# Optimization experiments

Hardware: AMD Instinct MI355X
Metric: run time of the kernel (lower is better)

## Reference

```python
import jax, jax.numpy as jnp
import numpy as np

S = 41          # seq_len
D_IN = 1280
D_OUT = 1024
HEADS = 4
HC = D_OUT // HEADS
EPS = 1e-5

# ---- static edge construction (faithful to the torch code, incl. duplicate edges) ----

def _local_edges(s, window=1):
    e = []
    for i in range(s):
        for j in range(max(0, i - window), min(s, i + window + 1)):
            if i != j:
                e += [(i, j), (j, i)]
    return np.array(e, dtype=np.int32).T

def _region_edges(s):
    e = []
    step = s // 3
    for st in range(0, s, step):
        blk = range(st, min(st + step, s))
        for i in blk:
            for j in blk:
                if i != j:
                    e += [(i, j), (j, i)]
    return np.array(e, dtype=np.int32).T

def _global_edges(s):
    r, c = np.triu_indices(s, 1)  # torch.combinations: (i, j) with i < j
    return np.stack([r, c]).astype(np.int32)

def _batch_edges(e, b, s):
    off = np.arange(b, dtype=np.int32) * s
    return (e[:, None, :] + off[None, :, None]).reshape(2, -1)

_LOCAL = _local_edges(S)
_REGION = _region_edges(S)
_GLOBAL = _global_edges(S)

# ---- layer primitives ----

def _layernorm(x, g, b):
    mu = x.mean(-1, keepdims=True)
    v = ((x - mu) ** 2).mean(-1, keepdims=True)
    return (x - mu) / jnp.sqrt(v + EPS) * g + b

def _gcn(x, w, b, src, tgt, n):
    # PyG GCNConv: x' = D^-1/2 (A + I) D^-1/2 (x W) + b
    h = x @ w
    sl = jnp.arange(n, dtype=src.dtype)
    s = jnp.concatenate([src, sl]); t = jnp.concatenate([tgt, sl])
    deg = jax.ops.segment_sum(jnp.ones(t.shape, h.dtype), t, n)
    dinv = jnp.where(deg > 0, jax.lax.rsqrt(jnp.maximum(deg, 1.0)), 0.0)
    norm = dinv[s] * dinv[t]
    return jax.ops.segment_sum(h[s] * norm[:, None], t, n) + b

def _gat(x, w, a_src, a_dst, b, src, tgt, n):
    # PyG GATConv (shared lin, self loops, leaky_relu 0.2, softmax over incoming edges)
    h = (x @ w).reshape(n, HEADS, HC)
    sl = jnp.arange(n, dtype=src.dtype)
    s = jnp.concatenate([src, sl]); t = jnp.concatenate([tgt, sl])
    al_s = (h * a_src).sum(-1)  # [n, H]
    al_d = (h * a_dst).sum(-1)
    e = jax.nn.leaky_relu(al_s[s] + al_d[t], 0.2)  # [E, H]
    m = jax.ops.segment_max(e, t, n)
    ex = jnp.exp(e - m[t])
    den = jax.ops.segment_sum(ex, t, n)
    alpha = ex / den[t]
    out = jax.ops.segment_sum(h[s] * alpha[:, :, None], t, n)
    return out.reshape(n, HEADS * HC) + b

def _sage(x, wl, bl, wr, src, tgt, n):
    # PyG SAGEConv: mean-aggregate neighbors, plus root transform
    cnt = jax.ops.segment_sum(jnp.ones(src.shape, x.dtype), tgt, n)
    agg = jax.ops.segment_sum(x[src], tgt, n) / jnp.maximum(cnt, 1.0)[:, None]
    return agg @ wl + bl + x @ wr


def setup_inputs() -> dict:
    key = jax.random.key(0)
    ks = jax.random.split(key, 16)
    sc = 0.02
    f32 = jnp.float32
    inp = {
        'x': jax.random.normal(ks[0], (512, S, D_IN), f32),
        'att_w': jax.random.normal(ks[1], (D_IN, 1), f32) * sc,
        'att_b': jnp.zeros((1,), f32),
        'gcn_w': jax.random.normal(ks[2], (D_IN, D_OUT), f32) * sc,
        'gcn_b': jnp.zeros((D_OUT,), f32),
        'sn_g': jnp.ones((D_OUT,), f32), 'sn_b': jnp.zeros((D_OUT,), f32),
        'gat_w': jax.random.normal(ks[3], (D_IN, D_OUT), f32) * sc,
        'gat_as': jax.random.normal(ks[4], (HEADS, HC), f32) * sc,
        'gat_ad': jax.random.normal(ks[5], (HEADS, HC), f32) * sc,
        'gat_b': jnp.zeros((D_OUT,), f32),
        'mn_g': jnp.ones((D_OUT,), f32), 'mn_b': jnp.zeros((D_OUT,), f32),
        'sage_wl': jax.random.normal(ks[6], (D_IN, D_OUT), f32) * sc,
        'sage_bl': jnp.zeros((D_OUT,), f32),
        'sage_wr': jax.random.normal(ks[7], (D_IN, D_OUT), f32) * sc,
        'fp_w1': jax.random.normal(ks[8], (D_IN, 512), f32) * sc,
        'fp_b1': jnp.zeros((512,), f32),
        'fp_w2': jax.random.normal(ks[9], (512, S), f32) * sc,
        'fp_b2': jnp.zeros((S,), f32),
        'dn_g': jnp.ones((D_OUT,), f32), 'dn_b': jnp.zeros((D_OUT,), f32),
        'gate_w': jax.random.normal(ks[10], (3 * D_OUT, 3), f32) * sc,
        'gate_b': jnp.zeros((3,), f32),
    }
    return inp


def reference(x, att_w, att_b, gcn_w, gcn_b, sn_g, sn_b, gat_w, gat_as, gat_ad, gat_b,
              mn_g, mn_b, sage_wl, sage_bl, sage_wr, fp_w1, fp_b1, fp_w2, fp_b2,
              dn_g, dn_b, gate_w, gate_b):
    B = x.shape[0]
    N = B * S
    le = jnp.asarray(_batch_edges(_LOCAL, B, S))
    re = jnp.asarray(_batch_edges(_REGION, B, S))
    ge = jnp.asarray(_batch_edges(_GLOBAL, B, S))

    xf = x.reshape(N, D_IN)
    # shallow: local gating -> GCN -> LN
    enhanced = xf * jax.nn.sigmoid(xf @ att_w + att_b)
    shallow = _gcn(enhanced, gcn_w, gcn_b, le[0], le[1], N)
    shallow = _layernorm(shallow.reshape(B, S, D_OUT), sn_g, sn_b)
    # medium: GAT over region blocks -> LN
    gat = _gat(xf, gat_w, gat_as[None], gat_ad[None], gat_b, re[0], re[1], N)
    gat = _layernorm(gat.reshape(B, S, D_OUT), mn_g, mn_b)
    # deep: learned propagation mixing, SAGE over global edges -> LN
    pw = jax.nn.softmax(jax.nn.relu(x @ fp_w1 + fp_b1) @ fp_w2 + fp_b2, axis=-1)  # [B,S,S]
    sage_in = jnp.einsum('bij,bjd->bid', pw, x).reshape(N, D_IN)
    sage = _sage(sage_in, sage_wl, sage_bl, sage_wr, ge[0], ge[1], N)
    sage = _layernorm(sage.reshape(B, S, D_OUT), dn_g, dn_b)
    # gated branch mixing
    combined = jnp.concatenate([shallow, gat, sage], axis=-1)
    gates = jax.nn.softmax(combined @ gate_w + gate_b, axis=-1)
    total = gates[..., 0:1] * shallow + gates[..., 1:2] * gat + gates[..., 2:3] * sage
    return (shallow, gat, total)
```

## Files before the change

### kernel.cpp

```cpp
#include <hip/hip_runtime.h>
#include <math.h>

static constexpr int S    = 41;
static constexpr int DIN  = 1280;
static constexpr int DOUT = 1024;
static constexpr int HEADS = 4;
static constexpr int HC   = 256;

typedef __attribute__((ext_vector_type(4))) float f32x4;
typedef __attribute__((ext_vector_type(8))) short short8;

__device__ __forceinline__ ushort f2bf(float f) {
  uint u = __float_as_uint(f);
  uint r = u + 0x7fffu + ((u >> 16) & 1u);
  return (ushort)(r >> 16);
}
__device__ __forceinline__ float bf2f(ushort u) {
  return __uint_as_float(((uint)u) << 16);
}

__device__ __forceinline__ void gload16(const ushort* g, ushort* l) {
  __builtin_amdgcn_global_load_lds((const __attribute__((address_space(1))) void*)g,
                                   (__attribute__((address_space(3))) void*)l, 16, 0, 0);
}

#define FENCE() asm volatile("" ::: "memory")


__device__ __forceinline__ float warpReduceSum(float v) {
#pragma unroll
  for (int off = 32; off; off >>= 1) v += __shfl_down(v, off);
  return v;
}


__global__ __launch_bounds__(256) void cvtsig_kernel(
    const float4* __restrict__ x, const float* __restrict__ att_w,
    const float* __restrict__ att_b, ushort4* __restrict__ xb, float* __restrict__ sig)
{
  int row  = blockIdx.x * 4 + (threadIdx.x >> 6);
  int lane = threadIdx.x & 63;
  const float4* xr = x + (size_t)row * (DIN / 4);
  const float4* wr = (const float4*)att_w;
  ushort4* xo = xb + (size_t)row * (DIN / 4);
  float acc = 0.f;
#pragma unroll
  for (int k = 0; k < DIN / 4 / 64; ++k) {
    float4 a = xr[lane + k * 64];
    float4 w = wr[lane + k * 64];
    acc += a.x * w.x + a.y * w.y + a.z * w.z + a.w * w.w;
    ushort4 o;
    o.x = f2bf(a.x); o.y = f2bf(a.y); o.z = f2bf(a.z); o.w = f2bf(a.w);
    xo[lane + k * 64] = o;
  }
  acc = warpReduceSum(acc);
  if (lane == 0) sig[row] = 1.f / (1.f + expf(-(acc + att_b[0])));
}


struct W4 { const float* src[4]; ushort* dst[4]; };

__global__ __launch_bounds__(256) void wcvt4_kernel(W4 w) {
  __shared__ float t[32][33];
  const float* W = w.src[blockIdx.z];
  ushort* out = w.dst[blockIdx.z];
  int n0 = blockIdx.x * 32, k0 = blockIdx.y * 32;
  int tx = threadIdx.x & 31, ty = threadIdx.x >> 5;
#pragma unroll
  for (int r = 0; r < 4; ++r) {
    int k = ty + r * 8;
    t[k][tx] = W[(size_t)(k0 + k) * DOUT + n0 + tx];
  }
  __syncthreads();
#pragma unroll
  for (int r = 0; r < 4; ++r) {
    int nn = ty + r * 8;
    out[(size_t)(n0 + nn) * DIN + k0 + tx] = f2bf(t[tx][nn]);
  }
}

__global__ __launch_bounds__(256) void wcvt_kernel(const float* __restrict__ W,
                                                   ushort* __restrict__ out,
                                                   int K, int N, int ostride, int koff) {
  __shared__ float t[32][33];
  int n0 = blockIdx.x * 32, k0 = blockIdx.y * 32;
  int tx = threadIdx.x & 31, ty = threadIdx.x >> 5;
#pragma unroll
  for (int r = 0; r < 4; ++r) {
    int k = ty + r * 8;
    t[k][tx] = W[(size_t)(k0 + k) * N + n0 + tx];
  }
  __syncthreads();
#pragma unroll
  for (int r = 0; r < 4; ++r) {
    int nn = ty + r * 8;
    out[(size_t)(n0 + nn) * ostride + koff + k0 + tx] = f2bf(t[tx][nn]);
  }
}

__global__ __launch_bounds__(256) void w2cvt_kernel(const float* __restrict__ w2,
                                                    ushort* __restrict__ wpw) {
  int idx = blockIdx.x * 256 + threadIdx.x;
  int n = idx >> 9, k = idx & 511;
  wpw[idx] = (n < S) ? f2bf(w2[(size_t)k * S + n]) : (ushort)0;
}


struct Epi {
  void* dst[5];
  const float* bias[5];
  int nend[5];
  int ld[5];
  int relu[5];
  const float* rs;
};


__global__ __launch_bounds__(512, 1) void gemm8p(
    const ushort* __restrict__ A, const ushort* __restrict__ Bt, int K, int nb, Epi e)
{
  __shared__ __align__(16) ushort As[4 * 8192];
  __shared__ __align__(16) ushort Bs[4 * 8192];

  int wg;
  {
    const int nwg = gridDim.x;
    const int bid = blockIdx.x;
    const int xcd = bid & 7, lin = bid >> 3;
    const int q = nwg >> 3, r = nwg & 7;
    wg = (xcd < r) ? (xcd * (q + 1) + lin) : (r * (q + 1) + (xcd - r) * q + lin);
  }
  const int bm = (wg / nb) * 256;
  const int bn = (wg % nb) * 256;

  const int tid  = threadIdx.x;
  const int wv   = tid >> 6;
  const int lane = tid & 63;
  const int l16  = lane & 15;
  const int l4   = lane >> 4;
  const int m0   = (wv >> 2) * 128;
  const int n0   = (wv & 3) * 64;

  const int rd0 = wv * 16 + (lane >> 2);
  const int rd1 = 128 + wv * 16 + (lane >> 2);
  const int cs0 = ((lane & 3) - ((rd0 >> 1) & 3)) & 3;
  const int cs1 = ((lane & 3) - ((rd1 >> 1) & 3)) & 3;

  const ushort* gA0 = A  + (size_t)(bm + rd0) * K + cs0 * 8;
  const ushort* gA1 = A  + (size_t)(bm + rd1) * K + cs1 * 8;
  const ushort* gB0 = Bt + (size_t)(bn + rd0) * K + cs0 * 8;
  const ushort* gB1 = Bt + (size_t)(bn + rd1) * K + cs1 * 8;

  auto stageA = [&](int h, int kof) {
    gload16(gA0 + kof, &As[h * 8192 + wv * 512]);
    gload16(gA1 + kof, &As[h * 8192 + (8 + wv) * 512]);
  };
  auto stageB = [&](int h, int kof) {
    gload16(gB0 + kof, &Bs[h * 8192 + wv * 512]);
    gload16(gB1 + kof, &Bs[h * 8192 + (8 + wv) * 512]);
  };

  const int rchunk = ((l4 + ((l16 >> 1) & 3)) & 3) * 8;

  f32x4 acc[8][4];
#pragma unroll
  for (int i = 0; i < 8; ++i)
#pragma unroll
    for (int j = 0; j < 4; ++j) acc[i][j] = (f32x4)0.f;

  const int NT = K >> 6;

  stageA(0, 0);  stageB(0, 0);
  stageA(1, 32); stageB(1, 32);
  stageA(2, 64); stageB(2, 64);
  asm volatile("s_waitcnt vmcnt(8)" ::: "memory");
  __builtin_amdgcn_s_barrier();
  FENCE();

  auto tileBody = [&](int T, const int db) {
    const int hA = db * 2;
    const int hB = db * 2 + 1;
    short8 a[4], b[4];

#pragma unroll
    for (int i = 0; i < 4; ++i)
      a[i] = *reinterpret_cast<const short8*>(&As[hA * 8192 + (m0 + i * 16 + l16) * 32 + rchunk]);
#pragma unroll
    for (int j = 0; j < 4; ++j)
      b[j] = *reinterpret_cast<const short8*>(&Bs[hA * 8192 + (n0 + j * 16 + l16) * 32 + rchunk]);
    if (T + 1 < NT) stageA((db ^ 1) * 2 + 1, (T + 1) * 64 + 32);
    FENCE(); __builtin_amdgcn_s_barrier(); FENCE();
    __builtin_amdgcn_s_setprio(1);
#pragma unroll
    for (int i = 0; i < 4; ++i)
#pragma unroll
      for (int j = 0; j < 4; ++j)
        acc[i][j] = __builtin_amdgcn_mfma_f32_16x16x32_bf16(a[i], b[j], acc[i][j], 0, 0, 0);
    __builtin_amdgcn_s_setprio(0);
    FENCE(); __builtin_amdgcn_s_barrier(); FENCE();

#pragma unroll
    for (int i = 0; i < 4; ++i)
      a[i] = *reinterpret_cast<const short8*>(&As[hA * 8192 + (m0 + 64 + i * 16 + l16) * 32 + rchunk]);
    if (T + 1 < NT) {
      stageB((db ^ 1) * 2 + 1, (T + 1) * 64 + 32);
      asm volatile("s_waitcnt vmcnt(8)" ::: "memory");
    } else {
      asm volatile("s_waitcnt vmcnt(0)" ::: "memory");
    }
    FENCE(); __builtin_amdgcn_s_barrier(); FENCE();
    __builtin_amdgcn_s_setprio(1);
#pragma unroll
    for (int i = 0; i < 4; ++i)
#pragma unroll
      for (int j = 0; j < 4; ++j)
        acc[4 + i][j] = __builtin_amdgcn_mfma_f32_16x16x32_bf16(a[i], b[j], acc[4 + i][j], 0, 0, 0);
    __builtin_amdgcn_s_setprio(0);
    FENCE(); __builtin_amdgcn_s_barrier(); FENCE();

#pragma unroll
    for (int i = 0; i < 4; ++i)
      a[i] = *reinterpret_cast<const short8*>(&As[hB * 8192 + (m0 + i * 16 + l16) * 32 + rchunk]);
#pragma unroll
    for (int j = 0; j < 4; ++j)
      b[j] = *reinterpret_cast<const short8*>(&Bs[hB * 8192 + (n0 + j * 16 + l16) * 32 + rchunk]);
    if (T + 2 < NT) stageA(hA, (T + 2) * 64);
    FENCE(); __builtin_amdgcn_s_barrier(); FENCE();
    __builtin_amdgcn_s_setprio(1);
#pragma unroll
    for (int i = 0; i < 4; ++i)
#pragma unroll
      for (int j = 0; j < 4; ++j)
        acc[i][j] = __builtin_amdgcn_mfma_f32_16x16x32_bf16(a[i], b[j], acc[i][j], 0, 0, 0);
    __builtin_amdgcn_s_setprio(0);
    FENCE(); __builtin_amdgcn_s_barrier(); FENCE();

#pragma unroll
    for (int i = 0; i < 4; ++i)
      a[i] = *reinterpret_cast<const short8*>(&As[hB * 8192 + (m0 + 64 + i * 16 + l16) * 32 + rchunk]);
    if (T + 2 < NT) {
      stageB(hA, (T + 2) * 64);
      asm volatile("s_waitcnt vmcnt(8)" ::: "memory");
    } else if (T + 1 < NT) {
      asm volatile("s_waitcnt vmcnt(4)" ::: "memory");
    }
    FENCE(); __builtin_amdgcn_s_barrier(); FENCE();
    __builtin_amdgcn_s_setprio(1);
#pragma unroll
    for (int i = 0; i < 4; ++i)
#pragma unroll
      for (int j = 0; j < 4; ++j)
        acc[4 + i][j] = __builtin_amdgcn_mfma_f32_16x16x32_bf16(a[i], b[j], acc[4 + i][j], 0, 0, 0);
    __builtin_amdgcn_s_setprio(0);
    FENCE(); __builtin_amdgcn_s_barrier(); FENCE();
  };

  for (int T = 0; T < NT; T += 2) {
    tileBody(T, 0);
    tileBody(T + 1, 1);
  }

  void* dstv; const float* bias; const float* rs = nullptr; int ldc, cb, relu;
  if (bn < e.nend[0])      { dstv = e.dst[0]; ldc = e.ld[0]; cb = bn;             bias = e.bias[0]; relu = e.relu[0]; rs = e.rs; }
  else if (bn < e.nend[1]) { dstv = e.dst[1]; ldc = e.ld[1]; cb = bn - e.nend[0]; bias = e.bias[1]; relu = e.relu[1]; }
  else if (bn < e.nend[2]) { dstv = e.dst[2]; ldc = e.ld[2]; cb = bn - e.nend[1]; bias = e.bias[2]; relu = e.relu[2]; }
  else if (bn < e.nend[3]) { dstv = e.dst[3]; ldc = e.ld[3]; cb = bn - e.nend[2]; bias = e.bias[3]; relu = e.relu[3]; }
  else                     { dstv = e.dst[4]; ldc = e.ld[4]; cb = bn - e.nend[3]; bias = e.bias[4]; relu = e.relu[4]; }

#pragma unroll
  for (int i = 0; i < 8; ++i) {
    int mbase = bm + m0 + i * 16 + l4 * 4;
    float rsv[4];
#pragma unroll
    for (int r = 0; r < 4; ++r) rsv[r] = rs ? rs[mbase + r] : 1.f;
#pragma unroll
    for (int j = 0; j < 4; ++j) {
      int col = cb + n0 + j * 16 + l16;
      float bv = bias ? bias[col] : 0.f;
#pragma unroll
      for (int r = 0; r < 4; ++r) {
        float t = acc[i][j][r] * rsv[r] + bv;
        if (relu) t = fmaxf(t, 0.f);
        ((ushort*)dstv)[(size_t)(mbase + r) * ldc + col] = f2bf(t);
      }
    }
  }
}


template<bool F32OUT>
__global__ __launch_bounds__(256) void gemm_bf16(
    const ushort* __restrict__ A, const ushort* __restrict__ Bt, int K, int nb, Epi e)
{
  __shared__ __align__(16) ushort As[3][128 * 32];
  __shared__ __align__(16) ushort Bs[3][128 * 32];

  const int bid = blockIdx.x;
  const int bm  = (bid / nb) * 128;
  const int bn  = (bid % nb) * 128;

  const int tid  = threadIdx.x;
  const int w    = tid >> 6;
  const int lane = tid & 63;
  const int l16  = lane & 15;
  const int l4   = lane >> 4;
  const int m0   = (w >> 1) * 64;
  const int n0   = (w & 1) * 64;

  const int rloc = lane >> 2;
  const int cpos = lane & 3;
  const int cdat = (cpos - (rloc >> 1)) & 3;
  const int srow = w * 32 + rloc;
  const int scol = cdat * 8;

  f32x4 acc[4][4];
#pragma unroll
  for (int i = 0; i < 4; ++i)
#pragma unroll
    for (int j = 0; j < 4; ++j) acc[i][j] = (f32x4)0.f;

  const ushort* pA0 = A  + (size_t)(bm + srow) * K + scol;
  const ushort* pA1 = A  + (size_t)(bm + srow + 16) * K + scol;
  const ushort* pB0 = Bt + (size_t)(bn + srow) * K + scol;
  const ushort* pB1 = Bt + (size_t)(bn + srow + 16) * K + scol;

  auto stage = [&](int buf, int kt) {
    gload16(pA0 + kt, &As[buf][w * 1024]);
    gload16(pA1 + kt, &As[buf][w * 1024 + 512]);
    gload16(pB0 + kt, &Bs[buf][w * 1024]);
    gload16(pB1 + kt, &Bs[buf][w * 1024 + 512]);
  };

  const int rchunk = ((l4 + (l16 >> 1)) & 3) * 8;

  const int nsteps = K >> 5;
  stage(0, 0); stage(1, 32); stage(2, 64);

  for (int t = 0; t < nsteps; ++t) {
    if (t == 0)                asm volatile("s_waitcnt vmcnt(8)" ::: "memory");
    else if (t == nsteps - 1)  asm volatile("s_waitcnt vmcnt(0)" ::: "memory");
    else                       asm volatile("s_waitcnt vmcnt(4)" ::: "memory");
    __builtin_amdgcn_s_barrier();
    FENCE();

    if (t >= 1 && t + 2 < nsteps) stage((t + 2) % 3, (t + 2) * 32);

    const int cur = t % 3;
    short8 a[4], b[4];
#pragma unroll
    for (int i = 0; i < 4; ++i)
      a[i] = *reinterpret_cast<const short8*>(&As[cur][(m0 + i * 16 + l16) * 32 + rchunk]);
#pragma unroll
    for (int j = 0; j < 4; ++j)
      b[j] = *reinterpret_cast<const short8*>(&Bs[cur][(n0 + j * 16 + l16) * 32 + rchunk]);
    __builtin_amdgcn_s_setprio(1);
#pragma unroll
    for (int i = 0; i < 4; ++i)
#pragma unroll
      for (int j = 0; j < 4; ++j)
        acc[i][j] = __builtin_amdgcn_mfma_f32_16x16x32_bf16(a[i], b[j], acc[i][j], 0, 0, 0);
    __builtin_amdgcn_s_setprio(0);
  }

  void* dstv; const float* bias; const float* rs = nullptr; int ldc, cb, relu;
  if (bn < e.nend[0])      { dstv = e.dst[0]; ldc = e.ld[0]; cb = bn;             bias = e.bias[0]; relu = e.relu[0]; rs = e.rs; }
  else if (bn < e.nend[1]) { dstv = e.dst[1]; ldc = e.ld[1]; cb = bn - e.nend[0]; bias = e.bias[1]; relu = e.relu[1]; }
  else if (bn < e.nend[2]) { dstv = e.dst[2]; ldc = e.ld[2]; cb = bn - e.nend[1]; bias = e.bias[2]; relu = e.relu[2]; }
  else if (bn < e.nend[3]) { dstv = e.dst[3]; ldc = e.ld[3]; cb = bn - e.nend[2]; bias = e.bias[3]; relu = e.relu[3]; }
  else                     { dstv = e.dst[4]; ldc = e.ld[4]; cb = bn - e.nend[3]; bias = e.bias[4]; relu = e.relu[4]; }

#pragma unroll
  for (int i = 0; i < 4; ++i) {
    int mbase = bm + m0 + i * 16 + l4 * 4;
    float rsv[4];
#pragma unroll
    for (int r = 0; r < 4; ++r) rsv[r] = rs ? rs[mbase + r] : 1.f;
#pragma unroll
    for (int j = 0; j < 4; ++j) {
      int col = cb + n0 + j * 16 + l16;
      float bv = bias ? bias[col] : 0.f;
#pragma unroll
      for (int r = 0; r < 4; ++r) {
        float t = acc[i][j][r] * rsv[r] + bv;
        if (relu) t = fmaxf(t, 0.f);
        if (F32OUT) ((float*)dstv)[(size_t)(mbase + r) * ldc + col] = t;
        else        ((ushort*)dstv)[(size_t)(mbase + r) * ldc + col] = f2bf(t);
      }
    }
  }
}


__global__ __launch_bounds__(256) void pwprep_kernel(
    const float* __restrict__ fp2, const float* __restrict__ fp_b2,
    float* __restrict__ pc)
{
  int b = blockIdx.x;
  int tid = threadIdx.x, wv = tid >> 6, lane = tid & 63;
  __shared__ float pws[S][S];
  for (int i = wv; i < S; i += 4) {
    float v = (lane < S) ? (fp2[(size_t)(b * S + i) * 128 + lane] + fp_b2[lane]) : -1e30f;
    float m = v;
#pragma unroll
    for (int off = 32; off; off >>= 1) m = fmaxf(m, __shfl_xor(m, off));
    float e = (lane < S) ? expf(v - m) : 0.f;
    float sum = e;
#pragma unroll
    for (int off = 32; off; off >>= 1) sum += __shfl_xor(sum, off);
    if (lane < S) {
      float p = e / sum;
      pws[i][lane] = p;
      pc[((size_t)b * S + i) * 128 + lane] = p;
    }
  }
  __syncthreads();
  if (tid < S) {
    float run = 0.f;
    for (int i = 0; i < S; ++i) {
      pc[((size_t)b * S + i) * 128 + 64 + tid] = (i > 0) ? run / (float)i : 0.f;
      run += pws[i][tid];
    }
  }
}


__global__ __launch_bounds__(256) void mixc_kernel(
    const float* __restrict__ pc, const ushort* __restrict__ xr,
    const ushort* __restrict__ xl, const float* __restrict__ sage_bl,
    ushort* __restrict__ hbuf)
{
  int b  = blockIdx.y;
  int d0 = blockIdx.x * 256;
  int tid = threadIdx.x;

  float xrv[S], xlv[S];
  const ushort* xrp = xr + (size_t)(b * S) * DOUT + d0 + tid;
  const ushort* xlp = xl + (size_t)(b * S) * DOUT + d0 + tid;
#pragma unroll
  for (int j = 0; j < S; ++j) {
    xrv[j] = bf2f(xrp[(size_t)j * DOUT]);
    xlv[j] = bf2f(xlp[(size_t)j * DOUT]);
  }
  float bl = sage_bl[d0 + tid];
  ushort* op = hbuf + (size_t)(b * S) * DOUT + d0 + tid;
  const float* pcb = pc + (size_t)(b * S) * 128;
  for (int i = 0; i < S; ++i) {
    const float* row = pcb + (size_t)i * 128;
    float acc = bl;
#pragma unroll
    for (int j = 0; j < S; ++j)
      acc += row[j] * xrv[j] + row[64 + j] * xlv[j];
    op[(size_t)i * DOUT] = f2bf(acc);
  }
}


__device__ __forceinline__ float dinv_local(int j) {
  return rsqrtf((j == 0 || j == S - 1) ? 3.f : 5.f);
}

__global__ __launch_bounds__(256) void tail_fused(
    const ushort* __restrict__ gcnh, const ushort* __restrict__ Cgat,
    const ushort* __restrict__ hbuf,
    const float* __restrict__ gcn_b, const float* __restrict__ sn_g, const float* __restrict__ sn_b,
    const float* __restrict__ gat_as, const float* __restrict__ gat_ad, const float* __restrict__ gat_b,
    const float* __restrict__ mn_g, const float* __restrict__ mn_b,
    const float* __restrict__ dn_g, const float* __restrict__ dn_b,
    const float* __restrict__ gw, const float* __restrict__ gb,
    float* __restrict__ out, int N)
{
  int b  = blockIdx.x >> 2;
  int rb = blockIdx.x & 3;
  int lo = rb * 13;
  int cnt = (rb < 3) ? 13 : 2;
  size_t OUT = (size_t)N * DOUT;
  int tid = threadIdx.x;
  int wv = tid >> 6, lane = tid & 63;
  int d0 = tid * 4;
  int head = tid >> 6;

  __shared__ __align__(16) ushort hs[13][DOUT];
  __shared__ float alpha[13][13][HEADS];
  __shared__ float als_l[13][HEADS], ald_l[13][HEADS];
  __shared__ float red6[2][6][4];
  __shared__ float red3[2][3][4];

  for (int r = 0; r < cnt; ++r) {
    const ushort4* src = (const ushort4*)(Cgat + (size_t)(b * S + lo + r) * DOUT);
    ((ushort4*)hs[r])[tid] = src[tid];
  }
  __syncthreads();

  {
    const float4* a4 = (const float4*)(gat_as + wv * HC);
    const float4* d4 = (const float4*)(gat_ad + wv * HC);
    float4 av = a4[lane], dv = d4[lane];
    for (int s = 0; s < cnt; ++s) {
      ushort4 hv4 = ((const ushort4*)&hs[s][wv * HC])[lane];
      float h0 = bf2f(hv4.x), h1 = bf2f(hv4.y), h2 = bf2f(hv4.z), h3 = bf2f(hv4.w);
      float a = h0 * av.x + h1 * av.y + h2 * av.z + h3 * av.w;
      float d = h0 * dv.x + h1 * dv.y + h2 * dv.z + h3 * dv.w;
      a = warpReduceSum(a);
      d = warpReduceSum(d);
      if (lane == 0) { als_l[s][wv] = a; ald_l[s][wv] = d; }
    }
  }
  __syncthreads();

  if (tid < cnt * HEADS) {
    int t = tid >> 2, hd = tid & 3;
    float myald = ald_l[t][hd];
    float m = -1e30f;
    for (int s = 0; s < cnt; ++s) {
      float v = als_l[s][hd] + myald;
      v = (v > 0.f) ? v : 0.2f * v;
      m = fmaxf(m, v);
    }
    float den = 0.f;
    for (int s = 0; s < cnt; ++s) {
      float v = als_l[s][hd] + myald;
      v = (v > 0.f) ? v : 0.2f * v;
      float ev = expf(v - m) * ((s == t) ? 1.f : 2.f);
      alpha[t][s][hd] = ev;
      den += ev;
    }
    float inv = 1.f / den;
    for (int s = 0; s < cnt; ++s) alpha[t][s][hd] *= inv;
  }
  __syncthreads();

  float4 gcnb4 = *(const float4*)(gcn_b + d0);
  float4 sng4  = *(const float4*)(sn_g + d0);
  float4 snb4  = *(const float4*)(sn_b + d0);
  float4 gatb4 = *(const float4*)(gat_b + d0);
  float4 mng4  = *(const float4*)(mn_g + d0);
  float4 mnb4  = *(const float4*)(mn_b + d0);
  float4 dng4  = *(const float4*)(dn_g + d0);
  float4 dnb4  = *(const float4*)(dn_b + d0);
  float gwsh[4][3], gwga[4][3], gwsa[4][3];
#pragma unroll
  for (int q = 0; q < 4; ++q)
#pragma unroll
    for (int c = 0; c < 3; ++c) {
      gwsh[q][c] = gw[(size_t)(d0 + q) * 3 + c];
      gwga[q][c] = gw[(size_t)(DOUT + d0 + q) * 3 + c];
      gwsa[q][c] = gw[(size_t)(2 * DOUT + d0 + q) * 3 + c];
    }

  for (int t = 0; t < cnt; ++t) {
    int i = lo + t;
    size_t n = (size_t)(b * S + i);
    int par = t & 1;

    float di = dinv_local(i);
    float wc = di * di;
    float wl = (i > 0)     ? 2.f * di * dinv_local(i - 1) : 0.f;
    float wr = (i < S - 1) ? 2.f * di * dinv_local(i + 1) : 0.f;
    const ushort* hc = gcnh + n * DOUT + d0;
    ushort4 c4  = *(const ushort4*)hc;
    ushort4 lft = (i > 0)     ? *(const ushort4*)(hc - DOUT) : ushort4{0, 0, 0, 0};
    ushort4 rgt = (i < S - 1) ? *(const ushort4*)(hc + DOUT) : ushort4{0, 0, 0, 0};
    const ushort* cp = (const ushort*)&c4;
    const ushort* lp = (const ushort*)&lft;
    const ushort* rp = (const ushort*)&rgt;
    const float* gbp = (const float*)&gcnb4;
    float sh[4];
#pragma unroll
    for (int q = 0; q < 4; ++q)
      sh[q] = wc * bf2f(cp[q]) + wl * bf2f(lp[q]) + wr * bf2f(rp[q]) + gbp[q];

    float ga[4] = {0.f, 0.f, 0.f, 0.f};
    for (int si = 0; si < cnt; ++si) {
      float aj = alpha[t][si][head];
      ushort4 hv = *(const ushort4*)&hs[si][d0];
      ga[0] += aj * bf2f(hv.x);
      ga[1] += aj * bf2f(hv.y);
      ga[2] += aj * bf2f(hv.z);
      ga[3] += aj * bf2f(hv.w);
    }
    const float* gab = (const float*)&gatb4;
#pragma unroll
    for (int q = 0; q < 4; ++q) ga[q] += gab[q];

    ushort4 s4v = *(const ushort4*)(hbuf + n * DOUT + d0);
    const ushort* sp = (const ushort*)&s4v;
    float sa[4];
#pragma unroll
    for (int q = 0; q < 4; ++q) sa[q] = bf2f(sp[q]);

    float red[6] = {0.f, 0.f, 0.f, 0.f, 0.f, 0.f};
#pragma unroll
    for (int q = 0; q < 4; ++q) {
      red[0] += sh[q]; red[1] += sh[q] * sh[q];
      red[2] += ga[q]; red[3] += ga[q] * ga[q];
      red[4] += sa[q]; red[5] += sa[q] * sa[q];
    }
#pragma unroll
    for (int r = 0; r < 6; ++r) red[r] = warpReduceSum(red[r]);
    if (lane == 0) {
#pragma unroll
      for (int r = 0; r < 6; ++r) red6[par][r][wv] = red[r];
    }
    __syncthreads();
#pragma unroll
    for (int r = 0; r < 6; ++r)
      red[r] = red6[par][r][0] + red6[par][r][1] + red6[par][r][2] + red6[par][r][3];

    float mu0 = red[0] * (1.f / DOUT), r0 = rsqrtf(red[1] * (1.f / DOUT) - mu0 * mu0 + 1e-5f);
    float mu1 = red[2] * (1.f / DOUT), r1 = rsqrtf(red[3] * (1.f / DOUT) - mu1 * mu1 + 1e-5f);
    float mu2 = red[4] * (1.f / DOUT), r2 = rsqrtf(red[5] * (1.f / DOUT) - mu2 * mu2 + 1e-5f);

    const float* sngp = (const float*)&sng4; const float* snbp = (const float*)&snb4;
    const float* mngp = (const float*)&mng4; const float* mnbp = (const float*)&mnb4;
    const float* dngp = (const float*)&dng4; const float* dnbp = (const float*)&dnb4;
    float shn[4], gan[4], san[4];
#pragma unroll
    for (int q = 0; q < 4; ++q) {
      shn[q] = (sh[q] - mu0) * r0 * sngp[q] + snbp[q];
      gan[q] = (ga[q] - mu1) * r1 * mngp[q] + mnbp[q];
      san[q] = (sa[q] - mu2) * r2 * dngp[q] + dnbp[q];
    }

    float p[3] = {0.f, 0.f, 0.f};
#pragma unroll
    for (int q = 0; q < 4; ++q) {
#pragma unroll
      for (int c = 0; c < 3; ++c)
        p[c] += shn[q] * gwsh[q][c] + gan[q] * gwga[q][c] + san[q] * gwsa[q][c];
    }
#pragma unroll
    for (int r = 0; r < 3; ++r) p[r] = warpReduceSum(p[r]);
    if (lane == 0) {
#pragma unroll
      for (int r = 0; r < 3; ++r) red3[par][r][wv] = p[r];
    }
    __syncthreads();
#pragma unroll
    for (int r = 0; r < 3; ++r)
      p[r] = red3[par][r][0] + red3[par][r][1] + red3[par][r][2] + red3[par][r][3];

    float l0 = p[0] + gb[0], l1 = p[1] + gb[1], l2 = p[2] + gb[2];
    float m = fmaxf(l0, fmaxf(l1, l2));
    float e0 = expf(l0 - m), e1 = expf(l1 - m), e2 = expf(l2 - m);
    float inv = 1.f / (e0 + e1 + e2);
    float g0 = e0 * inv, g1 = e1 * inv, g2 = e2 * inv;

    float4 o0, o1, o2;
    float* o0p = (float*)&o0; float* o1p = (float*)&o1; float* o2p = (float*)&o2;
#pragma unroll
    for (int q = 0; q < 4; ++q) {
      o0p[q] = shn[q];
      o1p[q] = gan[q];
      o2p[q] = g0 * shn[q] + g1 * gan[q] + g2 * san[q];
    }
    *(float4*)(out + n * DOUT + d0)           = o0;
    *(float4*)(out + OUT + n * DOUT + d0)     = o1;
    *(float4*)(out + 2 * OUT + n * DOUT + d0) = o2;
  }
}


extern "C" void kernel_launch(void* const* d_in, const int* in_sizes, int n_in,
                              void* d_out, int out_size, void* d_ws, size_t ws_size,
                              hipStream_t stream) {
  const float* x       = (const float*)d_in[0];
  const float* att_w   = (const float*)d_in[1];
  const float* att_b   = (const float*)d_in[2];
  const float* gcn_w   = (const float*)d_in[3];
  const float* gcn_b   = (const float*)d_in[4];
  const float* sn_g    = (const float*)d_in[5];
  const float* sn_b    = (const float*)d_in[6];
  const float* gat_w   = (const float*)d_in[7];
  const float* gat_as  = (const float*)d_in[8];
  const float* gat_ad  = (const float*)d_in[9];
  const float* gat_b   = (const float*)d_in[10];
  const float* mn_g    = (const float*)d_in[11];
  const float* mn_b    = (const float*)d_in[12];
  const float* sage_wl = (const float*)d_in[13];
  const float* sage_bl = (const float*)d_in[14];
  const float* sage_wr = (const float*)d_in[15];
  const float* fp_w1   = (const float*)d_in[16];
  const float* fp_b1   = (const float*)d_in[17];
  const float* fp_w2   = (const float*)d_in[18];
  const float* fp_b2   = (const float*)d_in[19];
  const float* dn_g    = (const float*)d_in[20];
  const float* dn_b    = (const float*)d_in[21];
  const float* gate_w  = (const float*)d_in[22];
  const float* gate_b  = (const float*)d_in[23];

  const int B = in_sizes[0] / (S * DIN);
  const int N = B * S;
  const int MB  = N / 128;
  const int MB2 = N / 256;
  const int NMEGA = 4608;
  float* out = (float*)d_out;

  char* ws = (char*)d_ws;
  size_t off = 0;
  auto alloc = [&](size_t bytes) { size_t p = off; off += (bytes + 255) & ~(size_t)255; return p; };
  ushort* xb   = (ushort*)(ws + alloc((size_t)N * DIN * 2));
  ushort* Bt   = (ushort*)(ws + alloc((size_t)NMEGA * DIN * 2));
  ushort* wpw  = (ushort*)(ws + alloc((size_t)128 * 512 * 2));
  ushort* gcnh = (ushort*)(ws + alloc((size_t)N * DOUT * 2));
  ushort* Cgat = (ushort*)(ws + alloc((size_t)N * DOUT * 2));
  ushort* xr   = (ushort*)(ws + alloc((size_t)N * DOUT * 2));
  ushort* xl   = (ushort*)(ws + alloc((size_t)N * DOUT * 2));
  ushort* hbuf = (ushort*)(ws + alloc((size_t)N * DOUT * 2));
  float*  fp2  = (float*)(ws + alloc((size_t)N * 128 * 4));
  float*  pc   = (float*)(ws + alloc((size_t)N * 128 * 4));
  float*  sig  = (float*)(ws + alloc((size_t)N * 4));
  ushort* fp1  = hbuf;

  dim3 blk(256);

  cvtsig_kernel<<<N / 4, blk, 0, stream>>>((const float4*)x, att_w, att_b, (ushort4*)xb, sig);
  W4 w4;
  w4.src[0] = gcn_w;  w4.dst[0] = Bt;
  w4.src[1] = gat_w;  w4.dst[1] = Bt + (size_t)1024 * DIN;
  w4.src[2] = sage_wr; w4.dst[2] = Bt + (size_t)2560 * DIN;
  w4.src[3] = sage_wl; w4.dst[3] = Bt + (size_t)3584 * DIN;
  wcvt4_kernel<<<dim3(DOUT / 32, DIN / 32, 4), blk, 0, stream>>>(w4);
  wcvt_kernel<<<dim3(512 / 32, DIN / 32), blk, 0, stream>>>(fp_w1, Bt + (size_t)2048 * DIN, DIN, 512, DIN, 0);
  w2cvt_kernel<<<dim3(128 * 512 / 256), blk, 0, stream>>>(fp_w2, wpw);

  Epi e1;
  e1.dst[0] = gcnh; e1.dst[1] = Cgat; e1.dst[2] = fp1; e1.dst[3] = xr; e1.dst[4] = xl;
  e1.bias[0] = nullptr; e1.bias[1] = nullptr; e1.bias[2] = fp_b1; e1.bias[3] = nullptr; e1.bias[4] = nullptr;
  e1.nend[0] = 1024; e1.nend[1] = 2048; e1.nend[2] = 2560; e1.nend[3] = 3584; e1.nend[4] = 4608;
  e1.ld[0] = DOUT; e1.ld[1] = DOUT; e1.ld[2] = 512; e1.ld[3] = DOUT; e1.ld[4] = DOUT;
  e1.relu[0] = 0; e1.relu[1] = 0; e1.relu[2] = 1; e1.relu[3] = 0; e1.relu[4] = 0;
  e1.rs = sig;
  gemm8p<<<dim3(MB2 * (NMEGA / 256)), dim3(512), 0, stream>>>(xb, Bt, DIN, NMEGA / 256, e1);

  Epi epw;
  epw.dst[0] = fp2; epw.dst[1] = nullptr; epw.dst[2] = nullptr; epw.dst[3] = nullptr; epw.dst[4] = nullptr;
  epw.bias[0] = nullptr; epw.bias[1] = nullptr; epw.bias[2] = nullptr; epw.bias[3] = nullptr; epw.bias[4] = nullptr;
  epw.nend[0] = 1 << 30; epw.nend[1] = 1 << 30; epw.nend[2] = 1 << 30; epw.nend[3] = 1 << 30; epw.nend[4] = 1 << 30;
  epw.ld[0] = 128; epw.ld[1] = 128; epw.ld[2] = 128; epw.ld[3] = 128; epw.ld[4] = 128;
  epw.relu[0] = 0; epw.relu[1] = 0; epw.relu[2] = 0; epw.relu[3] = 0; epw.relu[4] = 0;
  epw.rs = nullptr;
  gemm_bf16<true><<<dim3(MB), blk, 0, stream>>>(fp1, wpw, 512, 1, epw);

  pwprep_kernel<<<B, blk, 0, stream>>>(fp2, fp_b2, pc);
  mixc_kernel<<<dim3(DOUT / 256, B), blk, 0, stream>>>(pc, xr, xl, sage_bl, hbuf);

  tail_fused<<<B * 4, blk, 0, stream>>>(gcnh, Cgat, hbuf,
                                        gcn_b, sn_g, sn_b,
                                        gat_as, gat_ad, gat_b,
                                        mn_g, mn_b, dn_g, dn_b,
                                        gate_w, gate_b, out, N);
}
```

Baseline: 640.2 us.

## Process tail rows per wavefront to remove block-level barriers in reductions

The fused tail kernel now assigns whole rows to individual wavefronts, with each lane covering 16 columns. LayerNorm and gate reductions run entirely within a wave using xor shuffles, so the per-row shared-memory exchanges and two __syncthreads per row are gone. The cost is more registers per thread, parameter vectors reloaded inside the row loop, and uneven work across waves (13 rows over 4 waves, or only 2 rows in the last block).

```diff
diff --git a/kernel.cpp b/kernel.cpp
--- a/kernel.cpp
+++ b/kernel.cpp
@@ -30,6 +30,12 @@
 __device__ __forceinline__ float warpReduceSum(float v) {
 #pragma unroll
   for (int off = 32; off; off >>= 1) v += __shfl_down(v, off);
+  return v;
+}
+
+__device__ __forceinline__ float warpAllSum(float v) {
+#pragma unroll
+  for (int off = 32; off; off >>= 1) v += __shfl_xor(v, off);
   return v;
 }
 
@@ -475,15 +481,11 @@
   int cnt = (rb < 3) ? 13 : 2;
   size_t OUT = (size_t)N * DOUT;
   int tid = threadIdx.x;
-  int wv = tid >> 6, lane = tid & 63;
-  int d0 = tid * 4;
-  int head = tid >> 6;
+  int wvi = tid >> 6, lane = tid & 63;
 
   __shared__ __align__(16) ushort hs[13][DOUT];
   __shared__ float alpha[13][13][HEADS];
   __shared__ float als_l[13][HEADS], ald_l[13][HEADS];
-  __shared__ float red6[2][6][4];
-  __shared__ float red3[2][3][4];
 
   for (int r = 0; r < cnt; ++r) {
     const ushort4* src = (const ushort4*)(Cgat + (size_t)(b * S + lo + r) * DOUT);
@@ -492,17 +494,17 @@
   __syncthreads();
 
   {
-    const float4* a4 = (const float4*)(gat_as + wv * HC);
-    const float4* d4 = (const float4*)(gat_ad + wv * HC);
+    const float4* a4 = (const float4*)(gat_as + wvi * HC);
+    const float4* d4 = (const float4*)(gat_ad + wvi * HC);
     float4 av = a4[lane], dv = d4[lane];
     for (int s = 0; s < cnt; ++s) {
-      ushort4 hv4 = ((const ushort4*)&hs[s][wv * HC])[lane];
+      ushort4 hv4 = ((const ushort4*)&hs[s][wvi * HC])[lane];
       float h0 = bf2f(hv4.x), h1 = bf2f(hv4.y), h2 = bf2f(hv4.z), h3 = bf2f(hv4.w);
       float a = h0 * av.x + h1 * av.y + h2 * av.z + h3 * av.w;
       float d = h0 * dv.x + h1 * dv.y + h2 * dv.z + h3 * dv.w;
       a = warpReduceSum(a);
       d = warpReduceSum(d);
-      if (lane == 0) { als_l[s][wv] = a; ald_l[s][wv] = d; }
+      if (lane == 0) { als_l[s][wvi] = a; ald_l[s][wvi] = d; }
     }
   }
   __syncthreads();
@@ -529,133 +531,122 @@
   }
   __syncthreads();
 
-  float4 gcnb4 = *(const float4*)(gcn_b + d0);
-  float4 sng4  = *(const float4*)(sn_g + d0);
-  float4 snb4  = *(const float4*)(sn_b + d0);
-  float4 gatb4 = *(const float4*)(gat_b + d0);
-  float4 mng4  = *(const float4*)(mn_g + d0);
-  float4 mnb4  = *(const float4*)(mn_b + d0);
-  float4 dng4  = *(const float4*)(dn_g + d0);
-  float4 dnb4  = *(const float4*)(dn_b + d0);
-  float gwsh[4][3], gwga[4][3], gwsa[4][3];
-#pragma unroll
-  for (int q = 0; q < 4; ++q)
-#pragma unroll
-    for (int c = 0; c < 3; ++c) {
-      gwsh[q][c] = gw[(size_t)(d0 + q) * 3 + c];
-      gwga[q][c] = gw[(size_t)(DOUT + d0 + q) * 3 + c];
-      gwsa[q][c] = gw[(size_t)(2 * DOUT + d0 + q) * 3 + c];
-    }
-
-  for (int t = 0; t < cnt; ++t) {
+  for (int t = wvi; t < cnt; t += 4) {
     int i = lo + t;
     size_t n = (size_t)(b * S + i);
-    int par = t & 1;
 
     float di = dinv_local(i);
     float wc = di * di;
-    float wl = (i > 0)     ? 2.f * di * dinv_local(i - 1) : 0.f;
-    float wr = (i < S - 1) ? 2.f * di * dinv_local(i + 1) : 0.f;
-    const ushort* hc = gcnh + n * DOUT + d0;
-    ushort4 c4  = *(const ushort4*)hc;
-    ushort4 lft = (i > 0)     ? *(const ushort4*)(hc - DOUT) : ushort4{0, 0, 0, 0};
-    ushort4 rgt = (i < S - 1) ? *(const ushort4*)(hc + DOUT) : ushort4{0, 0, 0, 0};
-    const ushort* cp = (const ushort*)&c4;
-    const ushort* lp = (const ushort*)&lft;
-    const ushort* rp = (const ushort*)&rgt;
-    const float* gbp = (const float*)&gcnb4;
-    float sh[4];
-#pragma unroll
-    for (int q = 0; q < 4; ++q)
-      sh[q] = wc * bf2f(cp[q]) + wl * bf2f(lp[q]) + wr * bf2f(rp[q]) + gbp[q];
-
-    float ga[4] = {0.f, 0.f, 0.f, 0.f};
+    float wl_ = (i > 0)     ? 2.f * di * dinv_local(i - 1) : 0.f;
+    float wr_ = (i < S - 1) ? 2.f * di * dinv_local(i + 1) : 0.f;
+
+    float sh[4][4], ga[4][4], sa[4][4];
+    float red[6] = {0.f, 0.f, 0.f, 0.f, 0.f, 0.f};
+
+#pragma unroll
+    for (int q = 0; q < 4; ++q) {
+      int d0 = q * 256 + lane * 4;
+      const ushort* hc = gcnh + n * DOUT + d0;
+      ushort4 c4  = *(const ushort4*)hc;
+      ushort4 lft = (i > 0)     ? *(const ushort4*)(hc - DOUT) : ushort4{0, 0, 0, 0};
+      ushort4 rgt = (i < S - 1) ? *(const ushort4*)(hc + DOUT) : ushort4{0, 0, 0, 0};
+      float4 gb4 = *(const float4*)(gcn_b + d0);
+      const ushort* cp = (const ushort*)&c4;
+      const ushort* lp = (const ushort*)&lft;
+      const ushort* rp = (const ushort*)&rgt;
+      const float* gbp = (const float*)&gb4;
+#pragma unroll
+      for (int k = 0; k < 4; ++k)
+        sh[q][k] = wc * bf2f(cp[k]) + wl_ * bf2f(lp[k]) + wr_ * bf2f(rp[k]) + gbp[k];
+      ushort4 s4v = *(const ushort4*)(hbuf + n * DOUT + d0);
+      const ushort* sp = (const ushort*)&s4v;
+#pragma unroll
+      for (int k = 0; k < 4; ++k) sa[q][k] = bf2f(sp[k]);
+#pragma unroll
+      for (int k = 0; k < 4; ++k) ga[q][k] = 0.f;
+    }
+
     for (int si = 0; si < cnt; ++si) {
-      float aj = alpha[t][si][head];
-      ushort4 hv = *(const ushort4*)&hs[si][d0];
-      ga[0] += aj * bf2f(hv.x);
-      ga[1] += aj * bf2f(hv.y);
-      ga[2] += aj * bf2f(hv.z);
-      ga[3] += aj * bf2f(hv.w);
-    }
-    const float* gab = (const float*)&gatb4;
-#pragma unroll
-    for (int q = 0; q < 4; ++q) ga[q] += gab[q];
-
-    ushort4 s4v = *(const ushort4*)(hbuf + n * DOUT + d0);
-    const ushort* sp = (const ushort*)&s4v;
-    float sa[4];
-#pragma unroll
-    for (int q = 0; q < 4; ++q) sa[q] = bf2f(sp[q]);
-
-    float red[6] = {0.f, 0.f, 0.f, 0.f, 0.f, 0.f};
+      float4 al4 = *(const float4*)&alpha[t][si][0];
+      const float* alp = (const float*)&al4;
+#pragma unroll
+      for (int q = 0; q < 4; ++q) {
+        ushort4 hv = *(const ushort4*)&hs[si][q * 256 + lane * 4];
+        ga[q][0] += alp[q] * bf2f(hv.x);
+        ga[q][1] += alp[q] * bf2f(hv.y);
+        ga[q][2] += alp[q] * bf2f(hv.z);
+        ga[q][3] += alp[q] * bf2f(hv.w);
+      }
+    }
 #pragma unroll
     for (int q = 0; q < 4; ++q) {
-      red[0] += sh[q]; red[1] += sh[q] * sh[q];
-      red[2] += ga[q]; red[3] += ga[q] * ga[q];
-      red[4] += sa[q]; red[5] += sa[q] * sa[q];
-    }
-#pragma unroll
-    for (int r = 0; r < 6; ++r) red[r] = warpReduceSum(red[r]);
-    if (lane == 0) {
-#pragma unroll
-      for (int r = 0; r < 6; ++r) red6[par][r][wv] = red[r];
-    }
-    __syncthreads();
-#pragma unroll
-    for (int r = 0; r < 6; ++r)
-      red[r] = red6[par][r][0] + red6[par][r][1] + red6[par][r][2] + red6[par][r][3];
-
+      int d0 = q * 256 + lane * 4;
+      float4 gab4 = *(const float4*)(gat_b + d0);
+      const float* gab = (const float*)&gab4;
+#pragma unroll
+      for (int k = 0; k < 4; ++k) {
+        ga[q][k] += gab[k];
+        red[0] += sh[q][k]; red[1] += sh[q][k] * sh[q][k];
+        red[2] += ga[q][k]; red[3] += ga[q][k] * ga[q][k];
+        red[4] += sa[q][k]; red[5] += sa[q][k] * sa[q][k];
+      }
+    }
+#pragma unroll
+    for (int r = 0; r < 6; ++r) red[r] = warpAllSum(red[r]);
     float mu0 = red[0] * (1.f / DOUT), r0 = rsqrtf(red[1] * (1.f / DOUT) - mu0 * mu0 + 1e-5f);
     float mu1 = red[2] * (1.f / DOUT), r1 = rsqrtf(red[3] * (1.f / DOUT) - mu1 * mu1 + 1e-5f);
     float mu2 = red[4] * (1.f / DOUT), r2 = rsqrtf(red[5] * (1.f / DOUT) - mu2 * mu2 + 1e-5f);
 
-    const float* sngp = (const float*)&sng4; const float* snbp = (const float*)&snb4;
-    const float* mngp = (const float*)&mng4; const float* mnbp = (const float*)&mnb4;
-    const float* dngp = (const float*)&dng4; const float* dnbp = (const float*)&dnb4;
-    float shn[4], gan[4], san[4];
+    float p[3] = {0.f, 0.f, 0.f};
 #pragma unroll
     for (int q = 0; q < 4; ++q) {
-      shn[q] = (sh[q] - mu0) * r0 * sngp[q] + snbp[q];
-      gan[q] = (ga[q] - mu1) * r1 * mngp[q] + mnbp[q];
-      san[q] = (sa[q] - mu2) * r2 * dngp[q] + dnbp[q];
-    }
-
-    float p[3] = {0.f, 0.f, 0.f};
-#pragma unroll
-    for (int q = 0; q < 4; ++q) {
-#pragma unroll
-      for (int c = 0; c < 3; ++c)
-        p[c] += shn[q] * gwsh[q][c] + gan[q] * gwga[q][c] + san[q] * gwsa[q][c];
-    }
-#pragma unroll
-    for (int r = 0; r < 3; ++r) p[r] = warpReduceSum(p[r]);
-    if (lane == 0) {
-#pragma unroll
-      for (int r = 0; r < 3; ++r) red3[par][r][wv] = p[r];
-    }
-    __syncthreads();
-#pragma unroll
-    for (int r = 0; r < 3; ++r)
-      p[r] = red3[par][r][0] + red3[par][r][1] + red3[par][r][2] + red3[par][r][3];
-
+      int d0 = q * 256 + lane * 4;
+      float4 sng4 = *(const float4*)(sn_g + d0);
+      float4 snb4 = *(const float4*)(sn_b + d0);
+      float4 mng4 = *(const float4*)(mn_g + d0);
+      float4 mnb4 = *(const float4*)(mn_b + d0);
+      float4 dng4 = *(const float4*)(dn_g + d0);
+      float4 dnb4 = *(const float4*)(dn_b + d0);
+      const float* sngp = (const float*)&sng4; const float* snbp = (const float*)&snb4;
+      const float* mngp = (const float*)&mng4; const float* mnbp = (const float*)&mnb4;
+      const float* dngp = (const float*)&dng4; const float* dnbp = (const float*)&dnb4;
+#pragma unroll
+      for (int k = 0; k < 4; ++k) {
+        float shn = (sh[q][k] - mu0) * r0 * sngp[k] + snbp[k];
+        float gan = (ga[q][k] - mu1) * r1 * mngp[k] + mnbp[k];
+        float san = (sa[q][k] - mu2) * r2 * dngp[k] + dnbp[k];
+        sh[q][k] = shn; ga[q][k] = gan; sa[q][k] = san;
+        const float* w0 = gw + (size_t)(d0 + k) * 3;
+        const float* w1 = gw + (size_t)(DOUT + d0 + k) * 3;
+        const float* w2 = gw + (size_t)(2 * DOUT + d0 + k) * 3;
+#pragma unroll
+        for (int c = 0; c < 3; ++c)
+          p[c] += shn * w0[c] + gan * w1[c] + san * w2[c];
+      }
+    }
+#pragma unroll
+    for (int c = 0; c < 3; ++c) p[c] = warpAllSum(p[c]);
     float l0 = p[0] + gb[0], l1 = p[1] + gb[1], l2 = p[2] + gb[2];
     float m = fmaxf(l0, fmaxf(l1, l2));
     float e0 = expf(l0 - m), e1 = expf(l1 - m), e2 = expf(l2 - m);
     float inv = 1.f / (e0 + e1 + e2);
     float g0 = e0 * inv, g1 = e1 * inv, g2 = e2 * inv;
 
-    float4 o0, o1, o2;
-    float* o0p = (float*)&o0; float* o1p = (float*)&o1; float* o2p = (float*)&o2;
 #pragma unroll
     for (int q = 0; q < 4; ++q) {
-      o0p[q] = shn[q];
-      o1p[q] = gan[q];
-      o2p[q] = g0 * shn[q] + g1 * gan[q] + g2 * san[q];
-    }
-    *(float4*)(out + n * DOUT + d0)           = o0;
-    *(float4*)(out + OUT + n * DOUT + d0)     = o1;
-    *(float4*)(out + 2 * OUT + n * DOUT + d0) = o2;
+      int d0 = q * 256 + lane * 4;
+      float4 o0, o1, o2;
+      float* o0p = (float*)&o0; float* o1p = (float*)&o1; float* o2p = (float*)&o2;
+#pragma unroll
+      for (int k = 0; k < 4; ++k) {
+        o0p[k] = sh[q][k];
+        o1p[k] = ga[q][k];
+        o2p[k] = g0 * sh[q][k] + g1 * ga[q][k] + g2 * sa[q][k];
+      }
+      *(float4*)(out + n * DOUT + d0)           = o0;
+      *(float4*)(out + OUT + n * DOUT + d0)     = o1;
+      *(float4*)(out + 2 * OUT + n * DOUT + d0) = o2;
+    }
   }
 }
 
```

Measured after the change: 819.2 us. 1.28x slower.
